# Kernel tuning notes

Hardware: AMD Instinct MI355X
Metric: run time of the kernel (lower is better)

## Reference

```python
import jax, jax.numpy as jnp
import numpy as np

N, E, G = 100000, 1600000, 256
D, H, O, DEPTH = 128, 128, 128, 3
BN_EPS = 1e-5
LN_EPS = 1e-5


def setup_inputs() -> dict:
    key = jax.random.key(0)
    ks = jax.random.split(key, 16)
    x = jax.random.normal(ks[0], (N, D), dtype=jnp.float32)
    edge_index = jax.random.randint(ks[1], (2, E), 0, N, dtype=jnp.int64)
    batch = jnp.sort(jax.random.randint(ks[2], (N,), 0, G, dtype=jnp.int64))
    s1 = 1.0 / np.sqrt(D)
    s2 = 1.0 / np.sqrt(H)
    return {
        "x": x,
        "edge_index": edge_index,
        "batch": batch,
        "W1s": jax.random.normal(ks[3], (DEPTH, D, H), dtype=jnp.float32) * s1,
        "b1s": jax.random.normal(ks[4], (DEPTH, H), dtype=jnp.float32) * 0.01,
        "bn_g": jnp.ones((DEPTH, H), dtype=jnp.float32),
        "bn_b": jnp.zeros((DEPTH, H), dtype=jnp.float32),
        "bn_m": jax.random.normal(ks[5], (DEPTH, H), dtype=jnp.float32) * 0.1,
        "bn_v": jax.random.uniform(ks[6], (DEPTH, H), dtype=jnp.float32, minval=0.5, maxval=1.5),
        "W2s": jax.random.normal(ks[7], (DEPTH, H, H), dtype=jnp.float32) * s2,
        "b2s": jax.random.normal(ks[8], (DEPTH, H), dtype=jnp.float32) * 0.01,
        "Wp": jax.random.normal(ks[9], (H, O), dtype=jnp.float32) * s2,
        "bp": jax.random.normal(ks[10], (O,), dtype=jnp.float32) * 0.01,
        "ln_g": jnp.ones((O,), dtype=jnp.float32),
        "ln_b": jnp.zeros((O,), dtype=jnp.float32),
    }


def reference(x, edge_index, batch, W1s, b1s, bn_g, bn_b, bn_m, bn_v, W2s, b2s, Wp, bp, ln_g, ln_b):
    src, dst = edge_index[0], edge_index[1]
    h = x
    for l in range(DEPTH):
        # GIN aggregation (eps=0): (1+eps)*h_i + sum_{j->i} h_j
        agg = jax.ops.segment_sum(h[src], dst, num_segments=N)  # [N, H]
        z = h + agg
        # MLP: Linear -> BatchNorm(eval) -> ReLU -> Linear
        z = z @ W1s[l] + b1s[l]
        z = (z - bn_m[l]) * jax.lax.rsqrt(bn_v[l] + BN_EPS) * bn_g[l] + bn_b[l]
        z = jax.nn.relu(z)
        z = z @ W2s[l] + b2s[l]
        # post-conv ReLU (dropout = identity in eval)
        h = jax.nn.relu(z)
    # global mean pool over graphs
    counts = jax.ops.segment_sum(jnp.ones((N,), h.dtype), batch, num_segments=G)
    hg = jax.ops.segment_sum(h, batch, num_segments=G) / jnp.maximum(counts, 1.0)[:, None]
    # proj: Linear + LayerNorm
    p = hg @ Wp + bp
    mu = jnp.mean(p, axis=-1, keepdims=True)
    var = jnp.var(p, axis=-1, keepdims=True)
    return (p - mu) * jax.lax.rsqrt(var + LN_EPS) * ln_g + ln_b
```

## Files before the change

kernel.cpp:

```cpp
#include <hip/hip_runtime.h>
#include <hip/hip_bf16.h>


#define GDEPTH 3
#define CAP 64

typedef __bf16 bf16x8 __attribute__((ext_vector_type(8)));
typedef float  f32x4  __attribute__((ext_vector_type(4)));
typedef __hip_bfloat16  bf16;
typedef __hip_bfloat162 bf162;

#define CSR_CH 2048
#define NSLICE 8
#define NSLICE_LOG 3

__global__ void k_setup(const float* __restrict__ W1s, const float* __restrict__ W2s,
                        const float* __restrict__ b1s, const float* __restrict__ bng,
                        const float* __restrict__ bnb, const float* __restrict__ bnm,
                        const float* __restrict__ bnv,
                        bf16* __restrict__ Wp1, bf16* __restrict__ Wp2,
                        float* __restrict__ sArr, float* __restrict__ tArr,
                        const float4* __restrict__ x4, bf162* __restrict__ h,
                        const int* __restrict__ batch, int* __restrict__ gp,
                        const int* __restrict__ ei, int* __restrict__ fill,
                        int* __restrict__ col,
                        int N, int E, int G, int BCONV, int BGB, int BCSR) {
    int bid = blockIdx.x;
    int tid = threadIdx.x;
    if (bid % 3 == 0 && bid / 3 < BCSR) {
        int sb = bid / 3;
        int s = sb & (NSLICE - 1);
        int chunk = sb >> NSLICE_LOG;
        int lo = (int)((long long)s * N / NSLICE);
        int hi = (int)((long long)(s + 1) * N / NSLICE);
        int baseq = chunk * (CSR_CH / 4);
        const int4* d4p = (const int4*)(ei + E);
        const int4* s4p = (const int4*)ei;
        #pragma unroll
        for (int i = 0; i < CSR_CH / 1024; ++i) {
            int q = baseq + i * 256 + tid;
            int e0 = q * 4;
            if (e0 + 3 < E) {
                int4 d4 = d4p[q];
                if ((d4.x >= lo && d4.x < hi) || (d4.y >= lo && d4.y < hi) ||
                    (d4.z >= lo && d4.z < hi) || (d4.w >= lo && d4.w < hi)) {
                    int4 s4 = s4p[q];
                    if (d4.x >= lo && d4.x < hi) { int p = atomicAdd(&fill[d4.x], 1); if (p < CAP) col[(size_t)d4.x * CAP + p] = s4.x; }
                    if (d4.y >= lo && d4.y < hi) { int p = atomicAdd(&fill[d4.y], 1); if (p < CAP) col[(size_t)d4.y * CAP + p] = s4.y; }
                    if (d4.z >= lo && d4.z < hi) { int p = atomicAdd(&fill[d4.z], 1); if (p < CAP) col[(size_t)d4.z * CAP + p] = s4.z; }
                    if (d4.w >= lo && d4.w < hi) { int p = atomicAdd(&fill[d4.w], 1); if (p < CAP) col[(size_t)d4.w * CAP + p] = s4.w; }
                }
            } else if (e0 < E) {
                for (int e = e0; e < E; ++e) {
                    int d = ei[E + e];
                    if (d >= lo && d < hi) {
                        int p = atomicAdd(&fill[d], 1);
                        if (p < CAP) col[(size_t)d * CAP + p] = ei[e];
                    }
                }
            }
        }
        return;
    }
    {
        int nsc = (bid + 2) / 3;
        if (nsc > BCSR) nsc = BCSR;
        bid -= nsc;
    }
    if (bid < 384) {
        int idx = bid * 256 + tid;
        int l   = idx / 32768;
        int rem = idx - l * 32768;
        int w   = rem >> 14;
        int p   = rem & 16383;
        int j = p & 7, n = (p >> 3) & 127, tq = p >> 10;
        int quad = tq & 3, kk = tq >> 2;
        int k = kk * 32 + quad * 8 + j;
        const float* W = w ? W2s : W1s;
        bf16* Wp = w ? Wp2 : Wp1;
        Wp[l * 16384 + p] = __float2bfloat16(W[l * 16384 + k * 128 + n]);
        if (idx < GDEPTH * 128) {
            int ll = idx >> 7, c = idx & 127;
            float inv = rsqrtf(bnv[ll * 128 + c] + 1e-5f);
            float s = inv * bng[ll * 128 + c];
            sArr[idx] = s;
            tArr[idx] = (b1s[ll * 128 + c] - bnm[ll * 128 + c]) * s + bnb[ll * 128 + c];
        }
        return;
    }
    bid -= 384;
    if (bid < BCONV) {
        int i = bid * 256 + tid;
        int n4 = N * 32;
        if (i < n4) {
            float4 v = x4[i];
            bf162 a, b;
            a.x = __float2bfloat16(v.x); a.y = __float2bfloat16(v.y);
            b.x = __float2bfloat16(v.z); b.y = __float2bfloat16(v.w);
            h[2 * i] = a; h[2 * i + 1] = b;
        }
        return;
    }
    bid -= BCONV;
    if (bid < BGB) {
        int i = bid * 256 + tid;
        if (i < N) {
            int b = batch[i];
            if (i == 0) {
                for (int g = 0; g <= b; ++g) gp[g] = 0;
            } else {
                int pb = batch[i - 1];
                if (pb != b) for (int g = pb + 1; g <= b; ++g) gp[g] = i;
            }
            if (i == N - 1) {
                for (int g = b + 1; g <= G; ++g) gp[g] = N;
            }
        }
        return;
    }
}

__global__ __launch_bounds__(256) void k_layer(const bf16* __restrict__ h,
                                               const int* __restrict__ deg,
                                               const int* __restrict__ col,
                                               const bf16* __restrict__ Bp1,
                                               const bf16* __restrict__ Bp2,
                                               const float* __restrict__ sv,
                                               const float* __restrict__ tv,
                                               const float* __restrict__ b2,
                                               bf16* __restrict__ Out, int M) {
    __shared__ __align__(16) bf16 As[32 * 136];
    const int tid = threadIdx.x;
    const int m0 = blockIdx.x * 32;
    const int grp = tid >> 4, c = tid & 15;
    const bf16x8* h8 = (const bf16x8*)h;

    #pragma unroll
    for (int it = 0; it < 2; ++it) {
        int row = grp * 2 + it;
        int node = m0 + row;
        float acc[8];
        if (node < M) {
            bf16x8 self = h8[(size_t)node * 16 + c];
            #pragma unroll
            for (int k = 0; k < 8; ++k) acc[k] = (float)self[k];
            int d = deg[node]; if (d > CAP) d = CAP;
            const int* cb = col + (size_t)node * CAP;
            int e = 0;
            for (; e + 3 < d; e += 4) {
                int j0 = cb[e], j1 = cb[e + 1], j2 = cb[e + 2], j3 = cb[e + 3];
                bf16x8 v0 = h8[(size_t)j0 * 16 + c];
                bf16x8 v1 = h8[(size_t)j1 * 16 + c];
                bf16x8 v2 = h8[(size_t)j2 * 16 + c];
                bf16x8 v3 = h8[(size_t)j3 * 16 + c];
                #pragma unroll
                for (int k = 0; k < 8; ++k)
                    acc[k] += ((float)v0[k] + (float)v1[k]) + ((float)v2[k] + (float)v3[k]);
            }
            for (; e < d; ++e) {
                bf16x8 v = h8[(size_t)cb[e] * 16 + c];
                #pragma unroll
                for (int k = 0; k < 8; ++k) acc[k] += (float)v[k];
            }
        } else {
            #pragma unroll
            for (int k = 0; k < 8; ++k) acc[k] = 0.f;
        }
        bf16x8 r;
        #pragma unroll
        for (int k = 0; k < 8; ++k) {
            __hip_bfloat16 t = __float2bfloat16(acc[k]);
            r[k] = *(__bf16*)&t;
        }
        *(bf16x8*)(As + row * 136 + c * 8) = r;
    }
    __syncthreads();

    const int lane = tid & 63;
    const int wid = tid >> 6;
    const int wm = wid & 1, wn = wid >> 1;
    const int l15 = lane & 15, quad = lane >> 4;

    f32x4 acc[4];
    #pragma unroll
    for (int j = 0; j < 4; ++j) acc[j] = (f32x4){0.f, 0.f, 0.f, 0.f};
    #pragma unroll
    for (int kk = 0; kk < 4; ++kk) {
        bf16x8 a, b[4];
        #pragma unroll
        for (int tn = 0; tn < 4; ++tn)
            b[tn] = *(const bf16x8*)(Bp1 + ((kk * 4 + quad) * 128 + wn * 64 + tn * 16 + l15) * 8);
        a = *(const bf16x8*)(As + (wm * 16 + l15) * 136 + kk * 32 + quad * 8);
        #pragma unroll
        for (int tn = 0; tn < 4; ++tn)
            acc[tn] = __builtin_amdgcn_mfma_f32_16x16x32_bf16(a, b[tn], acc[tn], 0, 0, 0);
    }
    __syncthreads();
    #pragma unroll
    for (int tn = 0; tn < 4; ++tn) {
        int gc = wn * 64 + tn * 16 + l15;
        float scale = sv[gc], shift = tv[gc];
        #pragma unroll
        for (int r = 0; r < 4; ++r) {
            float v = fmaxf(acc[tn][r] * scale + shift, 0.f);
            int row = wm * 16 + quad * 4 + r;
            __hip_bfloat16 t = __float2bfloat16(v);
            As[row * 136 + gc] = *(bf16*)&t;
        }
    }
    __syncthreads();
    #pragma unroll
    for (int j = 0; j < 4; ++j) acc[j] = (f32x4){0.f, 0.f, 0.f, 0.f};
    #pragma unroll
    for (int kk = 0; kk < 4; ++kk) {
        bf16x8 a, b[4];
        #pragma unroll
        for (int tn = 0; tn < 4; ++tn)
            b[tn] = *(const bf16x8*)(Bp2 + ((kk * 4 + quad) * 128 + wn * 64 + tn * 16 + l15) * 8);
        a = *(const bf16x8*)(As + (wm * 16 + l15) * 136 + kk * 32 + quad * 8);
        #pragma unroll
        for (int tn = 0; tn < 4; ++tn)
            acc[tn] = __builtin_amdgcn_mfma_f32_16x16x32_bf16(a, b[tn], acc[tn], 0, 0, 0);
    }
    #pragma unroll
    for (int tn = 0; tn < 4; ++tn) {
        int gc = wn * 64 + tn * 16 + l15;
        float shift = b2[gc];
        #pragma unroll
        for (int r = 0; r < 4; ++r) {
            int gr = m0 + wm * 16 + quad * 4 + r;
            if (gr < M) {
                float v = fmaxf(acc[tn][r] + shift, 0.f);
                Out[(size_t)gr * 128 + gc] = __float2bfloat16(v);
            }
        }
    }
}

#define PCH 128
__global__ void k_pool(const bf16* __restrict__ h, const int* __restrict__ batch,
                       float* __restrict__ hga, int N) {
    int base = blockIdx.x * PCH;
    if (base >= N) return;
    int t = threadIdx.x;
    int end = base + PCH; if (end > N) end = N;
    int gcur = batch[base];
    float acc = 0.f;
    for (int i = base; i < end; ++i) {
        int g = batch[i];
        if (g != gcur) {
            atomicAdd(&hga[gcur * 128 + t], acc);
            acc = 0.f; gcur = g;
        }
        acc += __bfloat162float(h[(size_t)i * 128 + t]);
    }
    atomicAdd(&hga[gcur * 128 + t], acc);
}

__global__ void k_proj_ln(const float* __restrict__ hga, const int* __restrict__ gp,
                          const float* __restrict__ Wp,
                          const float* __restrict__ bp, const float* __restrict__ lng,
                          const float* __restrict__ lnb, float* __restrict__ out) {
    __shared__ float row[128];
    __shared__ float red[128];
    int g = blockIdx.x, t = threadIdx.x;
    int cntn = gp[g + 1] - gp[g];
    float inv = 1.0f / (float)(cntn < 1 ? 1 : cntn);
    row[t] = hga[g * 128 + t] * inv;
    __syncthreads();
    float p = bp[t];
    #pragma unroll 8
    for (int k = 0; k < 128; ++k) p += row[k] * Wp[k * 128 + t];
    red[t] = p; __syncthreads();
    for (int o = 64; o > 0; o >>= 1) { if (t < o) red[t] += red[t + o]; __syncthreads(); }
    float mu = red[0] * (1.0f / 128.0f);
    __syncthreads();
    float d = p - mu;
    red[t] = d * d; __syncthreads();
    for (int o = 64; o > 0; o >>= 1) { if (t < o) red[t] += red[t + o]; __syncthreads(); }
    float var = red[0] * (1.0f / 128.0f);
    out[g * 128 + t] = d * rsqrtf(var + 1e-5f) * lng[t] + lnb[t];
}

extern "C" void kernel_launch(void* const* d_in, const int* in_sizes, int n_in,
                              void* d_out, int out_size, void* d_ws, size_t ws_size,
                              hipStream_t stream) {
    const float* x   = (const float*)d_in[0];
    const int*   ei  = (const int*)d_in[1];
    const int*   bat = (const int*)d_in[2];
    const float* W1s = (const float*)d_in[3];
    const float* b1s = (const float*)d_in[4];
    const float* bng = (const float*)d_in[5];
    const float* bnb = (const float*)d_in[6];
    const float* bnm = (const float*)d_in[7];
    const float* bnv = (const float*)d_in[8];
    const float* W2s = (const float*)d_in[9];
    const float* b2s = (const float*)d_in[10];
    const float* Wp  = (const float*)d_in[11];
    const float* bp  = (const float*)d_in[12];
    const float* lng = (const float*)d_in[13];
    const float* lnb = (const float*)d_in[14];
    const int E = in_sizes[1] / 2;
    const int N = in_sizes[2];
    const int G = out_size / 128;

    char* w = (char*)d_ws;
    size_t off = 0;
    auto alloc = [&](size_t b) { char* p = w + off; off += (b + 255) & ~(size_t)255; return p; };
    bf16* buf_a = (bf16*)alloc((size_t)N * 128 * 2);
    bf16* buf_b = (bf16*)alloc((size_t)N * 128 * 2);
    int* col   = (int*)alloc(((size_t)N * CAP + 256) * 4);
    int* fill  = (int*)alloc((size_t)N * 4);
    int* gp    = (int*)alloc(2048);
    bf16* Wp1  = (bf16*)alloc((size_t)GDEPTH * 16384 * 2);
    bf16* Wp2  = (bf16*)alloc((size_t)GDEPTH * 16384 * 2);
    float* sA  = (float*)alloc((size_t)GDEPTH * 128 * 4);
    float* tA  = (float*)alloc((size_t)GDEPTH * 128 * 4);
    float* hga = (float*)alloc((size_t)G * 128 * 4);

    hipMemsetAsync(fill, 0, (size_t)N * 4, stream);
    hipMemsetAsync(hga, 0, (size_t)G * 128 * 4, stream);

    const int BCONV = (N * 32 + 255) / 256;
    const int BGB   = (N + 255) / 256;
    const int BCSR  = ((E + CSR_CH - 1) / CSR_CH) * NSLICE;
    k_setup<<<384 + BCONV + BGB + BCSR, 256, 0, stream>>>(
        W1s, W2s, b1s, bng, bnb, bnm, bnv, Wp1, Wp2, sA, tA,
        (const float4*)x, (bf162*)buf_a, bat, gp, ei, fill, col, N, E, G, BCONV, BGB, BCSR);

    const bf16* hcur = buf_a;
    bf16* hnext = buf_b;
    for (int l = 0; l < GDEPTH; ++l) {
        k_layer<<<(N + 31) / 32, 256, 0, stream>>>(hcur, fill, col,
                                                   Wp1 + (size_t)l * 16384,
                                                   Wp2 + (size_t)l * 16384,
                                                   sA + l * 128, tA + l * 128,
                                                   b2s + l * 128, hnext, N);
        bf16* tmp = hnext; hnext = (bf16*)hcur; hcur = tmp;
    }
    k_pool<<<(N + PCH - 1) / PCH, 128, 0, stream>>>(hcur, bat, hga, N);
    k_proj_ln<<<G, 128, 0, stream>>>(hga, gp, Wp, bp, lng, lnb, (float*)d_out);
}
```

Before: 475.9 us.

## Fuse mean pooling into projection/LayerNorm kernel using graph offsets

Removes the separate atomic-based pooling kernel and its zero-fill memset. Each graph's block now sums its own node rows directly, using the precomputed graph pointer array, before doing the projection and LayerNorm. This saves a launch, a memset and the atomics. The cost is that pooling parallelism drops to G=256 blocks of 256 threads, each reading about 390 rows serially, which could leave the GPU underused compared with the previous 782 blocks.

```diff
diff --git a/kernel.cpp b/kernel.cpp
--- a/kernel.cpp
+++ b/kernel.cpp
@@ -237,49 +237,47 @@
     }
 }
 
-#define PCH 128
-__global__ void k_pool(const bf16* __restrict__ h, const int* __restrict__ batch,
-                       float* __restrict__ hga, int N) {
-    int base = blockIdx.x * PCH;
-    if (base >= N) return;
-    int t = threadIdx.x;
-    int end = base + PCH; if (end > N) end = N;
-    int gcur = batch[base];
+__global__ __launch_bounds__(256) void k_proj_ln(const bf16* __restrict__ h,
+                                                 const int* __restrict__ gp,
+                                                 const float* __restrict__ Wp,
+                                                 const float* __restrict__ bp,
+                                                 const float* __restrict__ lng,
+                                                 const float* __restrict__ lnb,
+                                                 float* __restrict__ out) {
+    __shared__ float row[128];
+    __shared__ float red[256];
+    int g = blockIdx.x, tid = threadIdx.x;
+    int t = tid & 127, half = tid >> 7;
+    int lo = gp[g], hi = gp[g + 1];
     float acc = 0.f;
-    for (int i = base; i < end; ++i) {
-        int g = batch[i];
-        if (g != gcur) {
-            atomicAdd(&hga[gcur * 128 + t], acc);
-            acc = 0.f; gcur = g;
-        }
+    #pragma unroll 4
+    for (int i = lo + half; i < hi; i += 2)
         acc += __bfloat162float(h[(size_t)i * 128 + t]);
-    }
-    atomicAdd(&hga[gcur * 128 + t], acc);
-}
-
-__global__ void k_proj_ln(const float* __restrict__ hga, const int* __restrict__ gp,
-                          const float* __restrict__ Wp,
-                          const float* __restrict__ bp, const float* __restrict__ lng,
-                          const float* __restrict__ lnb, float* __restrict__ out) {
-    __shared__ float row[128];
-    __shared__ float red[128];
-    int g = blockIdx.x, t = threadIdx.x;
-    int cntn = gp[g + 1] - gp[g];
-    float inv = 1.0f / (float)(cntn < 1 ? 1 : cntn);
-    row[t] = hga[g * 128 + t] * inv;
-    __syncthreads();
-    float p = bp[t];
-    #pragma unroll 8
-    for (int k = 0; k < 128; ++k) p += row[k] * Wp[k * 128 + t];
-    red[t] = p; __syncthreads();
-    for (int o = 64; o > 0; o >>= 1) { if (t < o) red[t] += red[t + o]; __syncthreads(); }
+    red[tid] = acc;
+    __syncthreads();
+    if (tid < 128) {
+        int cnt = hi - lo;
+        float inv = 1.0f / (float)(cnt < 1 ? 1 : cnt);
+        row[t] = (red[t] + red[t + 128]) * inv;
+    }
+    __syncthreads();
+    float p = 0.f;
+    if (tid < 128) {
+        p = bp[t];
+        #pragma unroll 8
+        for (int k = 0; k < 128; ++k) p += row[k] * Wp[k * 128 + t];
+        red[t] = p;
+    }
+    __syncthreads();
+    for (int o = 64; o > 0; o >>= 1) { if (tid < o) red[tid] += red[tid + o]; __syncthreads(); }
     float mu = red[0] * (1.0f / 128.0f);
     __syncthreads();
-    float d = p - mu;
-    red[t] = d * d; __syncthreads();
-    for (int o = 64; o > 0; o >>= 1) { if (t < o) red[t] += red[t + o]; __syncthreads(); }
+    if (tid < 128) red[t] = (p - mu) * (p - mu);
+    __syncthreads();
+    for (int o = 64; o > 0; o >>= 1) { if (tid < o) red[tid] += red[tid + o]; __syncthreads(); }
     float var = red[0] * (1.0f / 128.0f);
-    out[g * 128 + t] = d * rsqrtf(var + 1e-5f) * lng[t] + lnb[t];
+    if (tid < 128)
+        out[g * 128 + t] = (p - mu) * rsqrtf(var + 1e-5f) * lng[t] + lnb[t];
 }
 
 extern "C" void kernel_launch(void* const* d_in, const int* in_sizes, int n_in,
@@ -316,10 +314,8 @@
     bf16* Wp2  = (bf16*)alloc((size_t)GDEPTH * 16384 * 2);
     float* sA  = (float*)alloc((size_t)GDEPTH * 128 * 4);
     float* tA  = (float*)alloc((size_t)GDEPTH * 128 * 4);
-    float* hga = (float*)alloc((size_t)G * 128 * 4);
 
     hipMemsetAsync(fill, 0, (size_t)N * 4, stream);
-    hipMemsetAsync(hga, 0, (size_t)G * 128 * 4, stream);
 
     const int BCONV = (N * 32 + 255) / 256;
     const int BGB   = (N + 255) / 256;
@@ -338,6 +334,5 @@
                                                    b2s + l * 128, hnext, N);
         bf16* tmp = hnext; hnext = (bf16*)hcur; hcur = tmp;
     }
-    k_pool<<<(N + PCH - 1) / PCH, 128, 0, stream>>>(hcur, bat, hga, N);
-    k_proj_ln<<<G, 128, 0, stream>>>(hga, gp, Wp, bp, lng, lnb, (float*)d_out);
+    k_proj_ln<<<G, 256, 0, stream>>>(hcur, gp, Wp, bp, lng, lnb, (float*)d_out);
 }
```

New measurement: 445.6 us. 1.07x faster.
